# Kernel tuning notes

Measured on AMD Instinct MI355X. Metric: run time of the kernel, lower is better.

## Reference

```python
import jax, jax.numpy as jnp
import numpy as np


def setup_inputs() -> dict:
    key = jax.random.key(0)
    k1, k2, k3 = jax.random.split(key, 3)
    B, Lc, Lq, D = 16, 1024, 1024, 256
    context_features = jax.random.normal(k1, (B, Lc, D), dtype=jnp.float32)
    question_features = jax.random.normal(k2, (B, Lq, D), dtype=jnp.float32)
    # nn.Linear(3D, 1, bias=False) weight, stored transposed as [3D, 1]
    weight = jax.random.normal(k3, (3 * D, 1), dtype=jnp.float32) * (1.0 / np.sqrt(3 * D))
    return {"context_features": context_features, "question_features": question_features, "weight": weight}


def reference(context_features, question_features, weight):
    # Trilinear similarity: sim[b,i,j] = [c_i ; q_j ; c_i*q_j] @ w
    # Decompose w = [wc ; wq ; wm] (each D) to avoid the O(B*Lc*Lq*3D) tensor:
    # sim = c@wc + q@wq + (c*wm) @ q^T   -- exact same math as the concat+Linear.
    D = context_features.shape[-1]
    w = weight[:, 0]
    wc, wq, wm = w[:D], w[D:2 * D], w[2 * D:]
    sim = (
        jnp.einsum('bcd,d->bc', context_features, wc)[:, :, None]
        + jnp.einsum('bqd,d->bq', question_features, wq)[:, None, :]
        + jnp.einsum('bcd,bqd->bcq', context_features * wm, question_features)
    )  # [B, Lc, Lq]
    weight_c2q = jax.nn.softmax(sim, axis=-1)                      # [B, Lc, Lq]
    c2q = jnp.einsum('bcq,bqd->bcd', weight_c2q, question_features)
    weight_q2c = jax.nn.softmax(jnp.max(sim, axis=2), axis=-1)     # [B, Lc]
    q2c = jnp.einsum('bc,bcd->bd', weight_q2c, context_features)   # [B, D]
    q2c = jnp.broadcast_to(q2c[:, None, :], c2q.shape)             # repeat over Lc
    return (c2q, q2c)
```

## Files before the change

kernel.cpp:

```cpp
#include <hip/hip_runtime.h>
#include <math.h>

#define BB 16
#define LC 1024
#define LQ 1024
#define DD 256

#define CTB 64
#define QTB 64
#define CM_S 264
#define QT_S 72

typedef __attribute__((ext_vector_type(4))) float f32x4;
typedef __attribute__((ext_vector_type(8))) short bf16x8;
typedef __attribute__((ext_vector_type(4))) short bf16x4;

__device__ inline short f2bf(float f) {
    union { float f; unsigned u; } v; v.f = f;
    unsigned r = v.u + 0x7FFFu + ((v.u >> 16) & 1u);
    return (short)(r >> 16);
}


__global__ __launch_bounds__(256) void k_terms(const float* __restrict__ ctx,
                                               const float* __restrict__ qst,
                                               const float* __restrict__ w,
                                               float* __restrict__ ws) {
    int gw = (blockIdx.x * 256 + threadIdx.x) >> 6;
    int lane = threadIdx.x & 63;
    bool isQ = gw >= BB * LC;
    int row = isQ ? gw - BB * LC : gw;
    const float* src = isQ ? qst : ctx;
    const float* wp  = isQ ? (w + DD) : w;
    float4 x  = *(const float4*)(src + (size_t)row * DD + lane * 4);
    float4 wv = *(const float4*)(wp + lane * 4);
    float d = x.x * wv.x + x.y * wv.y + x.z * wv.z + x.w * wv.w;
    #pragma unroll
    for (int off = 32; off; off >>= 1) d += __shfl_xor(d, off);
    float* dst = ws + (isQ ? 0 : BB * LQ);
    if (lane == 0) dst[row] = d;
}

__global__ __launch_bounds__(256, 1) void k_main(const float* __restrict__ ctx,
                                                 const float* __restrict__ qst,
                                                 const float* __restrict__ wght,
                                                 const float* __restrict__ ws,
                                                 float* __restrict__ out,
                                                 float* __restrict__ rowmax_out) {
    __shared__ short CMs[CTB][CM_S];
    __shared__ short Qs [QTB][CM_S];
    __shared__ short Qt [DD][QT_S];
    __shared__ short sP [CTB][QT_S];
    __shared__ float qtS[QTB];
    __shared__ float scaleS[CTB];
    __shared__ float sLinv[CTB];

    const int t  = threadIdx.x;
    const int l  = t & 63;
    const int wv = t >> 6;
    const int lx = l & 15;
    const int ls = l >> 4;
    const int b  = blockIdx.y;
    const int c0 = blockIdx.x * CTB;

    const float* qterm = ws;
    const float* cterm = ws + BB * LQ;

    #pragma unroll
    for (int kq = 0; kq < 4; ++kq) {
        #pragma unroll
        for (int jd = 0; jd < 4; ++jd) {
            int cl = 16 * wv + 4 * kq + ls;
            int d0 = 64 * jd + 4 * lx;
            const float4 x  = *(const float4*)(ctx + ((size_t)(b * LC + c0 + cl)) * DD + d0);
            const float4 wm = *(const float4*)(wght + 2 * DD + d0);
            bf16x4 o;
            o[0] = f2bf(x.x * wm.x); o[1] = f2bf(x.y * wm.y);
            o[2] = f2bf(x.z * wm.z); o[3] = f2bf(x.w * wm.w);
            *(bf16x4*)&CMs[cl][d0] = o;
        }
    }

    float mrun[4], lrun[4];
    f32x4 oacc[4][4];
    #pragma unroll
    for (int r = 0; r < 4; ++r) { mrun[r] = -1e30f; lrun[r] = 0.f; }
    #pragma unroll
    for (int cf = 0; cf < 4; ++cf)
        #pragma unroll
        for (int df = 0; df < 4; ++df)
            oacc[cf][df] = (f32x4){0.f, 0.f, 0.f, 0.f};

    for (int qt = 0; qt < LQ / QTB; ++qt) {
        __syncthreads();

        #pragma unroll
        for (int kq = 0; kq < 4; ++kq) {
            #pragma unroll
            for (int jd = 0; jd < 4; ++jd) {
                int ql = 16 * wv + 4 * kq + ls;
                int d0 = 64 * jd + 4 * lx;
                float4 x = *(const float4*)(qst + ((size_t)(b * LQ + qt * QTB + ql)) * DD + d0);
                bf16x4 o;
                o[0] = f2bf(x.x); o[1] = f2bf(x.y); o[2] = f2bf(x.z); o[3] = f2bf(x.w);
                *(bf16x4*)&Qs[ql][d0] = o;
                float X[4] = {x.x, x.y, x.z, x.w};
                float P1[4], X1[4], P2[4], X2[4];
                #pragma unroll
                for (int e = 0; e < 4; ++e) P1[e] = __shfl_xor(X[e ^ 1], 16);
                #pragma unroll
                for (int e = 0; e < 4; ++e) X1[e] = ((ls & 1) == (e & 1)) ? X[e] : P1[e];
                #pragma unroll
                for (int e = 0; e < 4; ++e) P2[e] = __shfl_xor(X1[e ^ 2], 32);
                #pragma unroll
                for (int e = 0; e < 4; ++e) X2[e] = ((ls & 2) == (e & 2)) ? X1[e] : P2[e];
                int dl = 64 * jd + 4 * lx + ls;
                bf16x4 ot;
                ot[0] = f2bf(X2[0]); ot[1] = f2bf(X2[1]); ot[2] = f2bf(X2[2]); ot[3] = f2bf(X2[3]);
                *(bf16x4*)&Qt[dl][16 * wv + 4 * kq] = ot;
            }
        }
        if (t < QTB) qtS[t] = qterm[b * LQ + qt * QTB + t];
        __syncthreads();

        f32x4 sacc[4];
        #pragma unroll
        for (int f = 0; f < 4; ++f) sacc[f] = (f32x4){0.f, 0.f, 0.f, 0.f};
        #pragma unroll
        for (int kk = 0; kk < 8; ++kk) {
            bf16x8 a = *(const bf16x8*)&CMs[16 * wv + lx][32 * kk + 8 * ls];
            #pragma unroll
            for (int f = 0; f < 4; ++f) {
                bf16x8 bq = *(const bf16x8*)&Qs[16 * f + lx][32 * kk + 8 * ls];
                sacc[f] = __builtin_amdgcn_mfma_f32_16x16x32_bf16(a, bq, sacc[f], 0, 0, 0);
            }
        }

        #pragma unroll
        for (int f = 0; f < 4; ++f) {
            float qv = qtS[16 * f + lx];
            #pragma unroll
            for (int r = 0; r < 4; ++r) sacc[f][r] += qv;
        }
        float scl[4];
        #pragma unroll
        for (int r = 0; r < 4; ++r) {
            float v = fmaxf(fmaxf(sacc[0][r], sacc[1][r]), fmaxf(sacc[2][r], sacc[3][r]));
            v = fmaxf(v, __shfl_xor(v, 1));
            v = fmaxf(v, __shfl_xor(v, 2));
            v = fmaxf(v, __shfl_xor(v, 4));
            v = fmaxf(v, __shfl_xor(v, 8));
            float mn = fmaxf(mrun[r], v);
            scl[r] = __expf(mrun[r] - mn);
            mrun[r] = mn;
            lrun[r] *= scl[r];
        }
        float p[4][4];
        float rs[4] = {0.f, 0.f, 0.f, 0.f};
        #pragma unroll
        for (int f = 0; f < 4; ++f)
            #pragma unroll
            for (int r = 0; r < 4; ++r) {
                p[f][r] = __expf(sacc[f][r] - mrun[r]);
                rs[r] += p[f][r];
            }
        #pragma unroll
        for (int r = 0; r < 4; ++r) {
            float v = rs[r];
            v += __shfl_xor(v, 1);
            v += __shfl_xor(v, 2);
            v += __shfl_xor(v, 4);
            v += __shfl_xor(v, 8);
            lrun[r] += v;
        }
        #pragma unroll
        for (int f = 0; f < 4; ++f)
            #pragma unroll
            for (int r = 0; r < 4; ++r)
                sP[16 * wv + 4 * ls + r][16 * f + lx] = f2bf(p[f][r]);
        if (lx == 0) {
            #pragma unroll
            for (int r = 0; r < 4; ++r) scaleS[16 * wv + 4 * ls + r] = scl[r];
        }
        __syncthreads();

        #pragma unroll
        for (int cf = 0; cf < 4; ++cf) {
            #pragma unroll
            for (int r = 0; r < 4; ++r) {
                float s = scaleS[16 * cf + 4 * ls + r];
                #pragma unroll
                for (int df = 0; df < 4; ++df) oacc[cf][df][r] *= s;
            }
        }
        #pragma unroll
        for (int kk = 0; kk < 2; ++kk) {
            bf16x8 pa[4];
            #pragma unroll
            for (int cf = 0; cf < 4; ++cf)
                pa[cf] = *(const bf16x8*)&sP[16 * cf + lx][32 * kk + 8 * ls];
            #pragma unroll
            for (int df = 0; df < 4; ++df) {
                bf16x8 qb = *(const bf16x8*)&Qt[64 * wv + 16 * df + lx][32 * kk + 8 * ls];
                #pragma unroll
                for (int cf = 0; cf < 4; ++cf)
                    oacc[cf][df] = __builtin_amdgcn_mfma_f32_16x16x32_bf16(pa[cf], qb, oacc[cf][df], 0, 0, 0);
            }
        }
    }

    if (lx == 0) {
        #pragma unroll
        for (int r = 0; r < 4; ++r) {
            int cl = 16 * wv + 4 * ls + r;
            sLinv[cl] = 1.0f / lrun[r];
            int c = b * LC + c0 + cl;
            rowmax_out[c] = mrun[r] + cterm[c];
        }
    }
    __syncthreads();
    #pragma unroll
    for (int cf = 0; cf < 4; ++cf) {
        #pragma unroll
        for (int r = 0; r < 4; ++r) {
            float li = sLinv[16 * cf + 4 * ls + r];
            size_t row = (size_t)(b * LC + c0 + 16 * cf + 4 * ls + r) * DD;
            #pragma unroll
            for (int df = 0; df < 4; ++df)
                out[row + 64 * wv + 16 * df + lx] = oacc[cf][df][r] * li;
        }
    }
}

__global__ __launch_bounds__(256) void k_q2c(const float* __restrict__ ctx,
                                             const float* __restrict__ rowmax,
                                             float* __restrict__ q2cvec) {
    __shared__ float sm[LC];
    __shared__ float red[256];
    int b = blockIdx.x;
    int chunk = blockIdx.y;
    int t = threadIdx.x;
    const float* rm = rowmax + b * LC;

    float lmax = -1e30f;
    #pragma unroll
    for (int k = 0; k < 4; ++k) {
        float v = rm[t + k * 256];
        sm[t + k * 256] = v;
        lmax = fmaxf(lmax, v);
    }
    red[t] = lmax;
    __syncthreads();
    for (int s = 128; s > 0; s >>= 1) {
        if (t < s) red[t] = fmaxf(red[t], red[t + s]);
        __syncthreads();
    }
    float gmax = red[0];
    __syncthreads();
    float lsum = 0.f;
    #pragma unroll
    for (int k = 0; k < 4; ++k) {
        int i = t + k * 256;
        float e = __expf(sm[i] - gmax);
        sm[i] = e;
        lsum += e;
    }
    red[t] = lsum;
    __syncthreads();
    for (int s = 128; s > 0; s >>= 1) {
        if (t < s) red[t] += red[t + s];
        __syncthreads();
    }
    float inv = 1.0f / red[0];

    int c0 = chunk * 32;
    float acc = 0.f;
    for (int c = c0; c < c0 + 32; ++c)
        acc += sm[c] * ctx[(size_t)(b * LC + c) * DD + t];
    atomicAdd(&q2cvec[b * DD + t], acc * inv);
}

__global__ __launch_bounds__(256) void k_bcast(const float* __restrict__ q2cvec,
                                               float* __restrict__ out2) {
    int g = blockIdx.x * 256 + threadIdx.x;
    int b  = g >> 16;
    int d4 = g & 63;
    ((float4*)out2)[g] = ((const float4*)q2cvec)[b * 64 + d4];
}

extern "C" void kernel_launch(void* const* d_in, const int* in_sizes, int n_in,
                              void* d_out, int out_size, void* d_ws, size_t ws_size,
                              hipStream_t stream) {
    const float* ctx = (const float*)d_in[0];
    const float* qst = (const float*)d_in[1];
    const float* w   = (const float*)d_in[2];
    float* out = (float*)d_out;
    float* ws  = (float*)d_ws;

    float* rowmax = ws + 32768;
    float* q2cvec = ws + 49152;

    hipMemsetAsync(q2cvec, 0, BB * DD * sizeof(float), stream);

    k_terms<<<(2 * BB * LC) / 4, 256, 0, stream>>>(ctx, qst, w, ws);

    k_main<<<dim3(LC / CTB, BB), 256, 0, stream>>>(ctx, qst, w, ws, out, rowmax);

    k_q2c<<<dim3(BB, 32), 256, 0, stream>>>(ctx, rowmax, q2cvec);

    k_bcast<<<(BB * LC * DD / 4) / 256, 256, 0, stream>>>(q2cvec, out + (size_t)BB * LC * DD);
}
```

Measured before the change: 184.1 us.

## Precompute bf16 Q and Q^T, split query tiles across two wave groups

A new prep kernel converts the question features to bf16 once, in both row-major and transposed layouts. It stores them in the second output buffer, which k_bcast overwrites later. k_main now uses 512 threads as two wave groups that each handle alternate query tiles, reading Q operands directly from global/L2 instead of converting them into LDS every tile. The two partial softmax states are merged through LDS at the end. This removes the redundant per-block conversion and transpose of Q across the 16 context blocks and doubles waves per block, at the cost of an extra kernel, direct global operand loads, and a merge step.

```diff
diff --git a/kernel.cpp b/kernel.cpp
--- a/kernel.cpp
+++ b/kernel.cpp
@@ -8,7 +8,6 @@
 
 #define CTB 64
 #define QTB 64
-#define CM_S 264
 #define QT_S 72
 
 typedef __attribute__((ext_vector_type(4))) float f32x4;
@@ -41,23 +40,72 @@
     if (lane == 0) dst[row] = d;
 }
 
-__global__ __launch_bounds__(256, 1) void k_main(const float* __restrict__ ctx,
-                                                 const float* __restrict__ qst,
-                                                 const float* __restrict__ wght,
-                                                 const float* __restrict__ ws,
-                                                 float* __restrict__ out,
-                                                 float* __restrict__ rowmax_out) {
-    __shared__ short CMs[CTB][CM_S];
-    __shared__ short Qs [QTB][CM_S];
-    __shared__ short Qt [DD][QT_S];
-    __shared__ short sP [CTB][QT_S];
-    __shared__ float qtS[QTB];
-    __shared__ float scaleS[CTB];
-    __shared__ float sLinv[CTB];
+__global__ __launch_bounds__(256) void k_prep(const float* __restrict__ qst,
+                                              short* __restrict__ Qbf,
+                                              short* __restrict__ Qtbf) {
+    __shared__ short Qt_lds[DD][QT_S];
+    int t = threadIdx.x;
+    int qt = blockIdx.x;
+    int b  = blockIdx.y;
+    int wv4 = t >> 6;
+    int l   = t & 63;
+    int lx  = l & 15;
+    int ls  = l >> 4;
+
+    #pragma unroll
+    for (int kq = 0; kq < 4; ++kq) {
+        #pragma unroll
+        for (int jd = 0; jd < 4; ++jd) {
+            int ql = 16 * wv4 + 4 * kq + ls;
+            int d0 = 64 * jd + 4 * lx;
+            float4 x = *(const float4*)(qst + ((size_t)(b * LQ + qt * QTB + ql)) * DD + d0);
+            bf16x4 o;
+            o[0] = f2bf(x.x); o[1] = f2bf(x.y); o[2] = f2bf(x.z); o[3] = f2bf(x.w);
+            *(bf16x4*)(Qbf + ((size_t)(b * LQ + qt * QTB + ql)) * DD + d0) = o;
+            float X[4] = {x.x, x.y, x.z, x.w};
+            float P1[4], X1[4], P2[4], X2[4];
+            #pragma unroll
+            for (int e = 0; e < 4; ++e) P1[e] = __shfl_xor(X[e ^ 1], 16);
+            #pragma unroll
+            for (int e = 0; e < 4; ++e) X1[e] = ((ls & 1) == (e & 1)) ? X[e] : P1[e];
+            #pragma unroll
+            for (int e = 0; e < 4; ++e) P2[e] = __shfl_xor(X1[e ^ 2], 32);
+            #pragma unroll
+            for (int e = 0; e < 4; ++e) X2[e] = ((ls & 2) == (e & 2)) ? X1[e] : P2[e];
+            int dl = 64 * jd + 4 * lx + ls;
+            bf16x4 ot;
+            ot[0] = f2bf(X2[0]); ot[1] = f2bf(X2[1]); ot[2] = f2bf(X2[2]); ot[3] = f2bf(X2[3]);
+            *(bf16x4*)&Qt_lds[dl][16 * wv4 + 4 * kq] = ot;
+        }
+    }
+    __syncthreads();
+    #pragma unroll
+    for (int rep = 0; rep < 8; ++rep) {
+        int d   = rep * 32 + (t >> 3);
+        int qch = t & 7;
+        bf16x8 v = *(const bf16x8*)&Qt_lds[d][8 * qch];
+        *(bf16x8*)(Qtbf + ((size_t)(b * DD + d)) * LQ + qt * QTB + 8 * qch) = v;
+    }
+}
+
+__global__ __launch_bounds__(512) void k_main(const float* __restrict__ ctx,
+                                              const short* __restrict__ Qbf,
+                                              const short* __restrict__ Qtbf,
+                                              const float* __restrict__ wght,
+                                              const float* __restrict__ ws,
+                                              float* __restrict__ out,
+                                              float* __restrict__ rowmax_out) {
+    __shared__ short CMp[4 * 8 * 512];
+    __shared__ short sPp[2][4 * 2 * 512];
+    __shared__ float scaleS[2][CTB];
+    __shared__ float mS[2][CTB], lS[2][CTB];
+    __shared__ float mergebuf[4 * 64 * 20];
 
     const int t  = threadIdx.x;
+    const int wv = t >> 6;
+    const int g  = wv >> 2;
+    const int w4 = wv & 3;
     const int l  = t & 63;
-    const int wv = t >> 6;
     const int lx = l & 15;
     const int ls = l >> 4;
     const int b  = blockIdx.y;
@@ -66,18 +114,23 @@
     const float* qterm = ws;
     const float* cterm = ws + BB * LQ;
 
-    #pragma unroll
-    for (int kq = 0; kq < 4; ++kq) {
-        #pragma unroll
-        for (int jd = 0; jd < 4; ++jd) {
-            int cl = 16 * wv + 4 * kq + ls;
-            int d0 = 64 * jd + 4 * lx;
-            const float4 x  = *(const float4*)(ctx + ((size_t)(b * LC + c0 + cl)) * DD + d0);
-            const float4 wm = *(const float4*)(wght + 2 * DD + d0);
-            bf16x4 o;
-            o[0] = f2bf(x.x * wm.x); o[1] = f2bf(x.y * wm.y);
-            o[2] = f2bf(x.z * wm.z); o[3] = f2bf(x.w * wm.w);
-            *(bf16x4*)&CMs[cl][d0] = o;
+    {
+        const int kh = g * 4;
+        int cl = 16 * w4 + lx;
+        #pragma unroll
+        for (int kq = 0; kq < 4; ++kq) {
+            int kk = kh + kq;
+            int d0 = 32 * kk + 8 * ls;
+            const float4 x0 = *(const float4*)(ctx + ((size_t)(b * LC + c0 + cl)) * DD + d0);
+            const float4 x1 = *(const float4*)(ctx + ((size_t)(b * LC + c0 + cl)) * DD + d0 + 4);
+            const float4 w0 = *(const float4*)(wght + 2 * DD + d0);
+            const float4 w1 = *(const float4*)(wght + 2 * DD + d0 + 4);
+            bf16x8 o;
+            o[0] = f2bf(x0.x * w0.x); o[1] = f2bf(x0.y * w0.y);
+            o[2] = f2bf(x0.z * w0.z); o[3] = f2bf(x0.w * w0.w);
+            o[4] = f2bf(x1.x * w1.x); o[5] = f2bf(x1.y * w1.y);
+            o[6] = f2bf(x1.z * w1.z); o[7] = f2bf(x1.w * w1.w);
+            *(bf16x8*)&CMp[(w4 * 8 + kk) * 512 + l * 8] = o;
         }
     }
 
@@ -91,56 +144,42 @@
         for (int df = 0; df < 4; ++df)
             oacc[cf][df] = (f32x4){0.f, 0.f, 0.f, 0.f};
 
-    for (int qt = 0; qt < LQ / QTB; ++qt) {
-        __syncthreads();
-
-        #pragma unroll
-        for (int kq = 0; kq < 4; ++kq) {
-            #pragma unroll
-            for (int jd = 0; jd < 4; ++jd) {
-                int ql = 16 * wv + 4 * kq + ls;
-                int d0 = 64 * jd + 4 * lx;
-                float4 x = *(const float4*)(qst + ((size_t)(b * LQ + qt * QTB + ql)) * DD + d0);
-                bf16x4 o;
-                o[0] = f2bf(x.x); o[1] = f2bf(x.y); o[2] = f2bf(x.z); o[3] = f2bf(x.w);
-                *(bf16x4*)&Qs[ql][d0] = o;
-                float X[4] = {x.x, x.y, x.z, x.w};
-                float P1[4], X1[4], P2[4], X2[4];
+    __syncthreads();
+
+    for (int it = 0; it < 8; ++it) {
+        const int qtile = 2 * it + g;
+        const size_t qbase = (size_t)b * LQ + qtile * QTB;
+
+        float qv[4];
+        #pragma unroll
+        for (int f = 0; f < 4; ++f) qv[f] = qterm[qbase + 16 * f + lx];
+
+        f32x4 sacc[4];
+        #pragma unroll
+        for (int f = 0; f < 4; ++f) sacc[f] = (f32x4){0.f, 0.f, 0.f, 0.f};
+        bf16x8 aP[2], bP[2][4];
+        aP[0] = *(const bf16x8*)&CMp[(w4 * 8 + 0) * 512 + l * 8];
+        #pragma unroll
+        for (int f = 0; f < 4; ++f)
+            bP[0][f] = *(const bf16x8*)(Qbf + (qbase + 16 * f + lx) * DD + 8 * ls);
+        #pragma unroll
+        for (int kk = 0; kk < 8; ++kk) {
+            int cur = kk & 1, nxt = cur ^ 1;
+            if (kk < 7) {
+                aP[nxt] = *(const bf16x8*)&CMp[(w4 * 8 + kk + 1) * 512 + l * 8];
                 #pragma unroll
-                for (int e = 0; e < 4; ++e) P1[e] = __shfl_xor(X[e ^ 1], 16);
-                #pragma unroll
-                for (int e = 0; e < 4; ++e) X1[e] = ((ls & 1) == (e & 1)) ? X[e] : P1[e];
-                #pragma unroll
-                for (int e = 0; e < 4; ++e) P2[e] = __shfl_xor(X1[e ^ 2], 32);
-                #pragma unroll
-                for (int e = 0; e < 4; ++e) X2[e] = ((ls & 2) == (e & 2)) ? X1[e] : P2[e];
-                int dl = 64 * jd + 4 * lx + ls;
-                bf16x4 ot;
-                ot[0] = f2bf(X2[0]); ot[1] = f2bf(X2[1]); ot[2] = f2bf(X2[2]); ot[3] = f2bf(X2[3]);
-                *(bf16x4*)&Qt[dl][16 * wv + 4 * kq] = ot;
-            }
-        }
-        if (t < QTB) qtS[t] = qterm[b * LQ + qt * QTB + t];
-        __syncthreads();
-
-        f32x4 sacc[4];
-        #pragma unroll
-        for (int f = 0; f < 4; ++f) sacc[f] = (f32x4){0.f, 0.f, 0.f, 0.f};
-        #pragma unroll
-        for (int kk = 0; kk < 8; ++kk) {
-            bf16x8 a = *(const bf16x8*)&CMs[16 * wv + lx][32 * kk + 8 * ls];
-            #pragma unroll
-            for (int f = 0; f < 4; ++f) {
-                bf16x8 bq = *(const bf16x8*)&Qs[16 * f + lx][32 * kk + 8 * ls];
-                sacc[f] = __builtin_amdgcn_mfma_f32_16x16x32_bf16(a, bq, sacc[f], 0, 0, 0);
-            }
+                for (int f = 0; f < 4; ++f)
+                    bP[nxt][f] = *(const bf16x8*)(Qbf + (qbase + 16 * f + lx) * DD + 32 * (kk + 1) + 8 * ls);
+            }
+            #pragma unroll
+            for (int f = 0; f < 4; ++f)
+                sacc[f] = __builtin_amdgcn_mfma_f32_16x16x32_bf16(aP[cur], bP[cur][f], sacc[f], 0, 0, 0);
         }
 
         #pragma unroll
         for (int f = 0; f < 4; ++f) {
-            float qv = qtS[16 * f + lx];
-            #pragma unroll
-            for (int r = 0; r < 4; ++r) sacc[f][r] += qv;
+            #pragma unroll
+            for (int r = 0; r < 4; ++r) sacc[f][r] += qv[f];
         }
         float scl[4];
         #pragma unroll
@@ -174,13 +213,18 @@
             lrun[r] += v;
         }
         #pragma unroll
-        for (int f = 0; f < 4; ++f)
-            #pragma unroll
-            for (int r = 0; r < 4; ++r)
-                sP[16 * wv + 4 * ls + r][16 * f + lx] = f2bf(p[f][r]);
+        for (int f = 0; f < 4; ++f) {
+            #pragma unroll
+            for (int r = 0; r < 4; ++r) {
+                int cl = 16 * w4 + 4 * ls + r;
+                int ql = 16 * f + lx;
+                int idx = ((cl >> 4) * 2 + (ql >> 5)) * 512 + ((cl & 15) + 16 * ((ql >> 3) & 3)) * 8 + (ql & 7);
+                sPp[g][idx] = f2bf(p[f][r]);
+            }
+        }
         if (lx == 0) {
             #pragma unroll
-            for (int r = 0; r < 4; ++r) scaleS[16 * wv + 4 * ls + r] = scl[r];
+            for (int r = 0; r < 4; ++r) scaleS[g][16 * w4 + 4 * ls + r] = scl[r];
         }
         __syncthreads();
 
@@ -188,46 +232,100 @@
         for (int cf = 0; cf < 4; ++cf) {
             #pragma unroll
             for (int r = 0; r < 4; ++r) {
-                float s = scaleS[16 * cf + 4 * ls + r];
+                float s = scaleS[g][16 * cf + 4 * ls + r];
                 #pragma unroll
                 for (int df = 0; df < 4; ++df) oacc[cf][df][r] *= s;
             }
         }
         #pragma unroll
         for (int kk = 0; kk < 2; ++kk) {
-            bf16x8 pa[4];
+            bf16x8 pa[4], qb[4];
             #pragma unroll
             for (int cf = 0; cf < 4; ++cf)
-                pa[cf] = *(const bf16x8*)&sP[16 * cf + lx][32 * kk + 8 * ls];
-            #pragma unroll
-            for (int df = 0; df < 4; ++df) {
-                bf16x8 qb = *(const bf16x8*)&Qt[64 * wv + 16 * df + lx][32 * kk + 8 * ls];
+                pa[cf] = *(const bf16x8*)&sPp[g][(cf * 2 + kk) * 512 + l * 8];
+            #pragma unroll
+            for (int df = 0; df < 4; ++df)
+                qb[df] = *(const bf16x8*)(Qtbf + ((size_t)(b * DD + 64 * w4 + 16 * df + lx)) * LQ
+                                          + qtile * QTB + 32 * kk + 8 * ls);
+            #pragma unroll
+            for (int df = 0; df < 4; ++df)
                 #pragma unroll
                 for (int cf = 0; cf < 4; ++cf)
-                    oacc[cf][df] = __builtin_amdgcn_mfma_f32_16x16x32_bf16(pa[cf], qb, oacc[cf][df], 0, 0, 0);
-            }
-        }
+                    oacc[cf][df] = __builtin_amdgcn_mfma_f32_16x16x32_bf16(pa[cf], qb[df], oacc[cf][df], 0, 0, 0);
+        }
+        __syncthreads();
     }
 
     if (lx == 0) {
         #pragma unroll
         for (int r = 0; r < 4; ++r) {
-            int cl = 16 * wv + 4 * ls + r;
-            sLinv[cl] = 1.0f / lrun[r];
-            int c = b * LC + c0 + cl;
-            rowmax_out[c] = mrun[r] + cterm[c];
-        }
-    }
-    __syncthreads();
+            mS[g][16 * w4 + 4 * ls + r] = mrun[r];
+            lS[g][16 * w4 + 4 * ls + r] = lrun[r];
+        }
+    }
+    __syncthreads();
+
+    float alpha[4][4], ltot[4][4], mtot[4][4];
     #pragma unroll
     for (int cf = 0; cf < 4; ++cf) {
         #pragma unroll
         for (int r = 0; r < 4; ++r) {
-            float li = sLinv[16 * cf + 4 * ls + r];
-            size_t row = (size_t)(b * LC + c0 + 16 * cf + 4 * ls + r) * DD;
+            int cl = 16 * cf + 4 * ls + r;
+            float m0 = mS[0][cl], m1 = mS[1][cl];
+            float mx = fmaxf(m0, m1);
+            float a0 = __expf(m0 - mx), a1 = __expf(m1 - mx);
+            mtot[cf][r] = mx;
+            ltot[cf][r] = a0 * lS[0][cl] + a1 * lS[1][cl];
+            alpha[cf][r] = (g == 0) ? a0 : a1;
+        }
+    }
+    #pragma unroll
+    for (int cf = 0; cf < 4; ++cf) {
+        #pragma unroll
+        for (int df = 0; df < 4; ++df)
+            #pragma unroll
+            for (int r = 0; r < 4; ++r)
+                oacc[cf][df][r] *= alpha[cf][r];
+    }
+    #pragma unroll
+    for (int cf = 0; cf < 4; ++cf) {
+        if (g == 1) {
             #pragma unroll
             for (int df = 0; df < 4; ++df)
-                out[row + 64 * wv + 16 * df + lx] = oacc[cf][df][r] * li;
+                *(f32x4*)&mergebuf[(w4 * 64 + l) * 20 + df * 4] = oacc[cf][df];
+        }
+        __syncthreads();
+        if (g == 0) {
+            #pragma unroll
+            for (int df = 0; df < 4; ++df) {
+                f32x4 v = *(const f32x4*)&mergebuf[(w4 * 64 + l) * 20 + df * 4];
+                oacc[cf][df][0] += v[0]; oacc[cf][df][1] += v[1];
+                oacc[cf][df][2] += v[2]; oacc[cf][df][3] += v[3];
+            }
+        }
+        __syncthreads();
+    }
+
+    if (g == 0) {
+        if (wv == 0 && lx == 0) {
+            #pragma unroll
+            for (int cf = 0; cf < 4; ++cf)
+                #pragma unroll
+                for (int r = 0; r < 4; ++r) {
+                    int c = b * LC + c0 + 16 * cf + 4 * ls + r;
+                    rowmax_out[c] = mtot[cf][r] + cterm[c];
+                }
+        }
+        #pragma unroll
+        for (int cf = 0; cf < 4; ++cf) {
+            #pragma unroll
+            for (int r = 0; r < 4; ++r) {
+                float inv = 1.0f / ltot[cf][r];
+                size_t row = (size_t)(b * LC + c0 + 16 * cf + 4 * ls + r) * DD;
+                #pragma unroll
+                for (int df = 0; df < 4; ++df)
+                    out[row + 64 * w4 + 16 * df + lx] = oacc[cf][df][r] * inv;
+            }
         }
     }
 }
@@ -294,19 +392,24 @@
     const float* ctx = (const float*)d_in[0];
     const float* qst = (const float*)d_in[1];
     const float* w   = (const float*)d_in[2];
-    float* out = (float*)d_out;
-    float* ws  = (float*)d_ws;
+    float* out  = (float*)d_out;
+    float* out2 = out + (size_t)BB * LC * DD;
+    float* ws   = (float*)d_ws;
 
     float* rowmax = ws + 32768;
     float* q2cvec = ws + 49152;
+    short* Qbf  = (short*)out2;
+    short* Qtbf = Qbf + (size_t)BB * LQ * DD;
 
     hipMemsetAsync(q2cvec, 0, BB * DD * sizeof(float), stream);
 
     k_terms<<<(2 * BB * LC) / 4, 256, 0, stream>>>(ctx, qst, w, ws);
 
-    k_main<<<dim3(LC / CTB, BB), 256, 0, stream>>>(ctx, qst, w, ws, out, rowmax);
+    k_prep<<<dim3(LQ / QTB, BB), 256, 0, stream>>>(qst, Qbf, Qtbf);
+
+    k_main<<<dim3(LC / CTB, BB), 512, 0, stream>>>(ctx, Qbf, Qtbf, w, ws, out, rowmax);
 
     k_q2c<<<dim3(BB, 32), 256, 0, stream>>>(ctx, rowmax, q2cvec);
 
-    k_bcast<<<(BB * LC * DD / 4) / 256, 256, 0, stream>>>(q2cvec, out + (size_t)BB * LC * DD);
-}
+    k_bcast<<<(BB * LC * DD / 4) / 256, 256, 0, stream>>>(q2cvec, out2);
+}
```

After: 197.8 us. 7.5% more time.
